# Kernel tuning notes

Hardware: AMD Instinct MI355X
Metric: run time of the kernel (lower is better)

Reference implementation:

```python
import jax, jax.numpy as jnp
import numpy as np


def setup_inputs() -> dict:
    key = jax.random.key(0)
    ks = jax.random.split(key, 7)
    n, L = 8, 1024
    s = 64            # input_size_1 = input_size_2 = 64
    d = s + 1         # 65, after bias-ones concat / h feature size
    inp = {
        "layer1": jax.random.normal(ks[0], (n, L, s), dtype=jnp.float32),
        "layer2": jax.random.normal(ks[1], (n, L, s), dtype=jnp.float32),
        "layer3": jax.random.normal(ks[2], (n, L, s), dtype=jnp.float32),
        "h1": jax.random.normal(ks[3], (n, L, d), dtype=jnp.float32),
        "h2": jax.random.normal(ks[4], (n, L, d), dtype=jnp.float32),
        "h3": jax.random.normal(ks[5], (n, L, d), dtype=jnp.float32),
        # quartic core W (xavier-normal-ish scale): shape (s1+1, s2+1, s2+1, s2+1)
        "W": jax.random.normal(ks[6], (d, d, d, d), dtype=jnp.float32) * 0.02,
    }
    return inp


def reference(layer1, layer2, layer3, h1, h2, h3, W):
    # Non-factorized, flag=True, 3D-input path of Qriaffine.forward:
    #   out = einsum('nia,abcd,njb,nic,njd->nij', [layer1;1], W, [layer2;1], h1, h2)
    # layer3 / h3 are unused in this branch (but layer3 is still concatenated
    # with ones in the original code, a no-op for the output).
    n, L, _ = layer1.shape
    ones = jnp.ones((n, L, 1), dtype=layer1.dtype)
    l1 = jnp.concatenate([layer1, ones], axis=-1)  # [n, L, d]
    l2 = jnp.concatenate([layer2, ones], axis=-1)  # [n, L, d]
    # efficient contraction order, avoiding the huge [n,L,d,d,d] intermediate:
    p = l1[..., :, None] * h1[..., None, :]          # niac: [n, L, d, d]
    q = jnp.einsum('niac,abcd->nibd', p, W)          # [n, L, d, d]
    r = l2[..., :, None] * h2[..., None, :]          # njbd: [n, L, d, d]
    out = jnp.einsum('nibd,njbd->nij', q, r)         # [n, L, L]
    return out
```

## Files before the change

kernel.cpp:

```cpp
#include <hip/hip_runtime.h>
#include <hip/hip_bf16.h>


typedef __attribute__((ext_vector_type(8))) short short8;
typedef __attribute__((ext_vector_type(16))) float floatx16;

#define KP 4288
#define DP 4352
#define NROW 8192

__device__ __forceinline__ void async_ld16(const void* g, void* l) {
  __builtin_amdgcn_global_load_lds(
      (const __attribute__((address_space(1))) unsigned int*)g,
      (__attribute__((address_space(3))) unsigned int*)l, 16, 0, 0);
}

__global__ void zero_kernel(float4* __restrict__ p, long n) {
  long i = (long)blockIdx.x * blockDim.x + threadIdx.x;
  long stride = (long)gridDim.x * blockDim.x;
  float4 z = make_float4(0.f, 0.f, 0.f, 0.f);
  for (; i < n; i += stride) p[i] = z;
}

__global__ void build_wt2(const float* __restrict__ W, __hip_bfloat16* __restrict__ Wt2) {
  __shared__ __hip_bfloat16 tile[65 * 66];
  const int a = blockIdx.x, b = blockIdx.y;
  const float* src = W + (size_t)(a * 65 + b) * 4225;
  for (int idx = threadIdx.x; idx < 4225; idx += 256) {
    int c = idx / 65, d = idx - c * 65;
    tile[d * 66 + c] = __float2bfloat16(src[idx]);
  }
  __syncthreads();
  for (int idx = threadIdx.x; idx < 4225; idx += 256) {
    int d = idx / 65, c = idx - d * 65;
    Wt2[(size_t)(b * 65 + d) * KP + a * 65 + c] = tile[d * 66 + c];
  }
}

__global__ void build_p(const float* __restrict__ layer, const float* __restrict__ h,
                        __hip_bfloat16* __restrict__ P, int width) {
  const int row = blockIdx.x;
  __shared__ float lv[65], hv[65];
  if (threadIdx.x < 64) lv[threadIdx.x] = layer[(size_t)row * 64 + threadIdx.x];
  if (threadIdx.x == 64) lv[64] = 1.0f;
  if (threadIdx.x < 65) hv[threadIdx.x] = h[(size_t)row * 65 + threadIdx.x];
  __syncthreads();
  for (int base = threadIdx.x * 8; base < width; base += 256 * 8) {
    alignas(16) __hip_bfloat16 tmp[8];
#pragma unroll
    for (int j = 0; j < 8; ++j) {
      int idx = base + j;
      float v = 0.f;
      if (idx < 4225) {
        int x = idx / 65, y = idx - x * 65;
        v = lv[x] * hv[y];
      }
      tmp[j] = __float2bfloat16(v);
    }
    *(float4*)(P + (size_t)row * width + base) = *(const float4*)tmp;
  }
}

template <int STORE_BF16>
__global__ __launch_bounds__(256) void gemm_nt(
    const __hip_bfloat16* __restrict__ A, const __hip_bfloat16* __restrict__ B,
    void* __restrict__ Cv, int K, int lda, int ldb, int ldc,
    long sA, long sB, long sC) {
  __shared__ alignas(16) __hip_bfloat16 As[128 * 64];
  __shared__ alignas(16) __hip_bfloat16 Bs[128 * 64];
  const int z = blockIdx.z;
  A += (long)z * sA;
  B += (long)z * sB;
  const int bm = blockIdx.y * 128;
  const int bn = blockIdx.x * 128;
  const int t = threadIdx.x;
  const int lane = t & 63;
  const int wave = t >> 6;
  const int l31 = lane & 31;
  const int lhi = lane >> 5;
  const int wm = (wave >> 1) * 64;
  const int wn = (wave & 1) * 64;

  const __hip_bfloat16* gA[4];
  const __hip_bfloat16* gB[4];
  __hip_bfloat16* lA[4];
  __hip_bfloat16* lB[4];
#pragma unroll
  for (int r = 0; r < 4; ++r) {
    int L = r * 256 + t;
    int row = L >> 3, sl = L & 7;
    int sg = sl ^ (row & 7);
    gA[r] = A + (size_t)(bm + row) * lda + sg * 8;
    gB[r] = B + (size_t)(bn + row) * ldb + sg * 8;
    lA[r] = As + (size_t)(r * 256 + wave * 64) * 8;
    lB[r] = Bs + (size_t)(r * 256 + wave * 64) * 8;
  }

  const int x7 = l31 & 7;
  const int rA0 = (wm + l31) * 64, rA1 = (wm + 32 + l31) * 64;
  const int rB0 = (wn + l31) * 64, rB1 = (wn + 32 + l31) * 64;

  floatx16 acc[2][2] = {};

  for (int k0 = 0; k0 < K; k0 += 64) {
    __syncthreads();
#pragma unroll
    for (int r = 0; r < 4; ++r) {
      async_ld16(gA[r] + k0, lA[r]);
      async_ld16(gB[r] + k0, lB[r]);
    }
    __syncthreads();

#pragma unroll
    for (int ks = 0; ks < 4; ++ks) {
      const int pc = ((ks * 2 + lhi) ^ x7) * 8;
      short8 a0 = *(const short8*)(&As[rA0 + pc]);
      short8 a1 = *(const short8*)(&As[rA1 + pc]);
      short8 b0 = *(const short8*)(&Bs[rB0 + pc]);
      short8 b1 = *(const short8*)(&Bs[rB1 + pc]);
      acc[0][0] = __builtin_amdgcn_mfma_f32_32x32x16_bf16(a0, b0, acc[0][0], 0, 0, 0);
      acc[0][1] = __builtin_amdgcn_mfma_f32_32x32x16_bf16(a0, b1, acc[0][1], 0, 0, 0);
      acc[1][0] = __builtin_amdgcn_mfma_f32_32x32x16_bf16(a1, b0, acc[1][0], 0, 0, 0);
      acc[1][1] = __builtin_amdgcn_mfma_f32_32x32x16_bf16(a1, b1, acc[1][1], 0, 0, 0);
    }
  }

  if (STORE_BF16) {
    __hip_bfloat16* C = (__hip_bfloat16*)Cv + (long)z * sC;
#pragma unroll
    for (int mt = 0; mt < 2; ++mt)
#pragma unroll
      for (int nt = 0; nt < 2; ++nt)
#pragma unroll
        for (int reg = 0; reg < 16; ++reg) {
          int row = bm + wm + mt * 32 + (reg & 3) + 8 * (reg >> 2) + 4 * lhi;
          int col = bn + wn + nt * 32 + l31;
          C[(size_t)row * ldc + col] = __float2bfloat16(acc[mt][nt][reg]);
        }
  } else {
    float* C = (float*)Cv + (long)z * sC;
#pragma unroll
    for (int mt = 0; mt < 2; ++mt)
#pragma unroll
      for (int nt = 0; nt < 2; ++nt)
#pragma unroll
        for (int reg = 0; reg < 16; ++reg) {
          int row = bm + wm + mt * 32 + (reg & 3) + 8 * (reg >> 2) + 4 * lhi;
          int col = bn + wn + nt * 32 + l31;
          C[(size_t)row * ldc + col] = acc[mt][nt][reg];
        }
  }
}

extern "C" void kernel_launch(void* const* d_in, const int* in_sizes, int n_in,
                              void* d_out, int out_size, void* d_ws, size_t ws_size,
                              hipStream_t stream) {
  const float* layer1 = (const float*)d_in[0];
  const float* layer2 = (const float*)d_in[1];
  const float* h1 = (const float*)d_in[3];
  const float* h2 = (const float*)d_in[4];
  const float* W = (const float*)d_in[6];
  float* out = (float*)d_out;

  char* ws = (char*)d_ws;
  __hip_bfloat16* P = (__hip_bfloat16*)(ws);
  __hip_bfloat16* Wt2 = (__hip_bfloat16*)(ws + 70254592ULL);
  __hip_bfloat16* Q = (__hip_bfloat16*)(ws + 107577344ULL);
  __hip_bfloat16* R = (__hip_bfloat16*)(ws);

  zero_kernel<<<2048, 256, 0, stream>>>((float4*)Wt2, (long)DP * KP * 2 / 16);
  build_wt2<<<dim3(65, 65), 256, 0, stream>>>(W, Wt2);
  build_p<<<NROW, 256, 0, stream>>>(layer1, h1, P, KP);
  gemm_nt<1><<<dim3(DP / 128, NROW / 128, 1), 256, 0, stream>>>(
      P, Wt2, Q, KP, KP, KP, DP, 0, 0, 0);
  build_p<<<NROW, 256, 0, stream>>>(layer2, h2, R, DP);
  gemm_nt<0><<<dim3(1024 / 128, 1024 / 128, 8), 256, 0, stream>>>(
      Q, R, out, DP, DP, DP, 1024, 1024L * DP, 1024L * DP, 1024L * 1024);
}
```

Measured before the change: 612.1 us.

## Pre-swizzle operands into MFMA fragment layout and load directly from global

```diff
diff --git a/kernel.cpp b/kernel.cpp
--- a/kernel.cpp
+++ b/kernel.cpp
@@ -8,12 +8,8 @@
 #define KP 4288
 #define DP 4352
 #define NROW 8192
-
-__device__ __forceinline__ void async_ld16(const void* g, void* l) {
-  __builtin_amdgcn_global_load_lds(
-      (const __attribute__((address_space(1))) unsigned int*)g,
-      (__attribute__((address_space(3))) unsigned int*)l, 16, 0, 0);
-}
+#define K16P 268
+#define K16D 272
 
 __global__ void zero_kernel(float4* __restrict__ p, long n) {
   long i = (long)blockIdx.x * blockDim.x + threadIdx.x;
@@ -22,123 +18,122 @@
   for (; i < n; i += stride) p[i] = z;
 }
 
-__global__ void build_wt2(const float* __restrict__ W, __hip_bfloat16* __restrict__ Wt2) {
-  __shared__ __hip_bfloat16 tile[65 * 66];
+__global__ void build_wt2f(const float* __restrict__ W, __hip_bfloat16* __restrict__ Bf) {
   const int a = blockIdx.x, b = blockIdx.y;
   const float* src = W + (size_t)(a * 65 + b) * 4225;
   for (int idx = threadIdx.x; idx < 4225; idx += 256) {
     int c = idx / 65, d = idx - c * 65;
-    tile[d * 66 + c] = __float2bfloat16(src[idx]);
-  }
-  __syncthreads();
-  for (int idx = threadIdx.x; idx < 4225; idx += 256) {
-    int d = idx / 65, c = idx - d * 65;
-    Wt2[(size_t)(b * 65 + d) * KP + a * 65 + c] = tile[d * 66 + c];
+    int bd = b * 65 + d;
+    int ac = a * 65 + c;
+    int lanef = (bd & 31) + ((ac >> 3) & 1) * 32;
+    size_t e = ((size_t)((bd >> 5) * K16P + (ac >> 4)) * 64 + lanef) * 8 + (ac & 7);
+    Bf[e] = __float2bfloat16(src[idx]);
   }
 }
 
-__global__ void build_p(const float* __restrict__ layer, const float* __restrict__ h,
-                        __hip_bfloat16* __restrict__ P, int width) {
-  const int row = blockIdx.x;
-  __shared__ float lv[65], hv[65];
-  if (threadIdx.x < 64) lv[threadIdx.x] = layer[(size_t)row * 64 + threadIdx.x];
-  if (threadIdx.x == 64) lv[64] = 1.0f;
-  if (threadIdx.x < 65) hv[threadIdx.x] = h[(size_t)row * 65 + threadIdx.x];
+__global__ void build_pf(const float* __restrict__ layer, const float* __restrict__ h,
+                         __hip_bfloat16* __restrict__ Pf, int K16) {
+  const int rb = blockIdx.x;
+  const int r0 = rb * 32;
+  __shared__ float lv[32][65];
+  __shared__ float hv[32][65];
+  const int t = threadIdx.x;
+  for (int i = t; i < 32 * 64; i += 256)
+    lv[i >> 6][i & 63] = layer[(size_t)(r0 + (i >> 6)) * 64 + (i & 63)];
+  if (t < 32) lv[t][64] = 1.0f;
+  for (int i = t; i < 32 * 65; i += 256) {
+    int rr = i / 65, y = i - rr * 65;
+    hv[rr][y] = h[(size_t)(r0 + rr) * 65 + y];
+  }
   __syncthreads();
-  for (int base = threadIdx.x * 8; base < width; base += 256 * 8) {
+  const int lane = t & 63;
+  const int rl = lane & 31;
+  const int kh = lane >> 5;
+  for (int kc = t >> 6; kc < K16; kc += 4) {
     alignas(16) __hip_bfloat16 tmp[8];
 #pragma unroll
-    for (int j = 0; j < 8; ++j) {
-      int idx = base + j;
+    for (int e = 0; e < 8; ++e) {
+      int k = kc * 16 + kh * 8 + e;
       float v = 0.f;
-      if (idx < 4225) {
-        int x = idx / 65, y = idx - x * 65;
-        v = lv[x] * hv[y];
+      if (k < 4225) {
+        int x = k / 65, y = k - x * 65;
+        v = lv[rl][x] * hv[rl][y];
       }
-      tmp[j] = __float2bfloat16(v);
+      tmp[e] = __float2bfloat16(v);
     }
-    *(float4*)(P + (size_t)row * width + base) = *(const float4*)tmp;
+    *(float4*)(Pf + ((size_t)(rb * K16 + kc) * 64 + lane) * 8) = *(const float4*)tmp;
   }
 }
 
-template <int STORE_BF16>
-__global__ __launch_bounds__(256) void gemm_nt(
+extern __shared__ char smem_[];
+template <int STORE_FRAG>
+__global__ __launch_bounds__(256, 2) void gemm_frag(
     const __hip_bfloat16* __restrict__ A, const __hip_bfloat16* __restrict__ B,
-    void* __restrict__ Cv, int K, int lda, int ldb, int ldc,
-    long sA, long sB, long sC) {
-  __shared__ alignas(16) __hip_bfloat16 As[128 * 64];
-  __shared__ alignas(16) __hip_bfloat16 Bs[128 * 64];
+    void* __restrict__ Cv, int K16, int cparam, long sA, long sB, long sC) {
   const int z = blockIdx.z;
-  A += (long)z * sA;
-  B += (long)z * sB;
-  const int bm = blockIdx.y * 128;
-  const int bn = blockIdx.x * 128;
+  const __hip_bfloat16* Ab = A + (size_t)z * sA;
+  const __hip_bfloat16* Bb = B + (size_t)z * sB;
   const int t = threadIdx.x;
   const int lane = t & 63;
   const int wave = t >> 6;
-  const int l31 = lane & 31;
-  const int lhi = lane >> 5;
-  const int wm = (wave >> 1) * 64;
-  const int wn = (wave & 1) * 64;
-
-  const __hip_bfloat16* gA[4];
-  const __hip_bfloat16* gB[4];
-  __hip_bfloat16* lA[4];
-  __hip_bfloat16* lB[4];
-#pragma unroll
-  for (int r = 0; r < 4; ++r) {
-    int L = r * 256 + t;
-    int row = L >> 3, sl = L & 7;
-    int sg = sl ^ (row & 7);
-    gA[r] = A + (size_t)(bm + row) * lda + sg * 8;
-    gB[r] = B + (size_t)(bn + row) * ldb + sg * 8;
-    lA[r] = As + (size_t)(r * 256 + wave * 64) * 8;
-    lB[r] = Bs + (size_t)(r * 256 + wave * 64) * 8;
-  }
-
-  const int x7 = l31 & 7;
-  const int rA0 = (wm + l31) * 64, rA1 = (wm + 32 + l31) * 64;
-  const int rB0 = (wn + l31) * 64, rB1 = (wn + 32 + l31) * 64;
+  const size_t rbA = (size_t)blockIdx.y * 4 + (wave >> 1) * 2;
+  const size_t rbB = (size_t)blockIdx.x * 4 + (wave & 1) * 2;
+  const __hip_bfloat16* pA0 = Ab + (rbA * K16 * 64 + lane) * 8;
+  const __hip_bfloat16* pA1 = pA0 + (size_t)K16 * 512;
+  const __hip_bfloat16* pB0 = Bb + (rbB * K16 * 64 + lane) * 8;
+  const __hip_bfloat16* pB1 = pB0 + (size_t)K16 * 512;
 
   floatx16 acc[2][2] = {};
 
-  for (int k0 = 0; k0 < K; k0 += 64) {
-    __syncthreads();
-#pragma unroll
-    for (int r = 0; r < 4; ++r) {
-      async_ld16(gA[r] + k0, lA[r]);
-      async_ld16(gB[r] + k0, lB[r]);
-    }
-    __syncthreads();
-
+  for (int kc = 0; kc < K16; kc += 4) {
+    const size_t off = (size_t)kc * 512;
+    short8 a0[4], a1[4], b0[4], b1[4];
 #pragma unroll
     for (int ks = 0; ks < 4; ++ks) {
-      const int pc = ((ks * 2 + lhi) ^ x7) * 8;
-      short8 a0 = *(const short8*)(&As[rA0 + pc]);
-      short8 a1 = *(const short8*)(&As[rA1 + pc]);
-      short8 b0 = *(const short8*)(&Bs[rB0 + pc]);
-      short8 b1 = *(const short8*)(&Bs[rB1 + pc]);
-      acc[0][0] = __builtin_amdgcn_mfma_f32_32x32x16_bf16(a0, b0, acc[0][0], 0, 0, 0);
-      acc[0][1] = __builtin_amdgcn_mfma_f32_32x32x16_bf16(a0, b1, acc[0][1], 0, 0, 0);
-      acc[1][0] = __builtin_amdgcn_mfma_f32_32x32x16_bf16(a1, b0, acc[1][0], 0, 0, 0);
-      acc[1][1] = __builtin_amdgcn_mfma_f32_32x32x16_bf16(a1, b1, acc[1][1], 0, 0, 0);
+      a0[ks] = *(const short8*)(pA0 + off + ks * 512);
+      a1[ks] = *(const short8*)(pA1 + off + ks * 512);
+      b0[ks] = *(const short8*)(pB0 + off + ks * 512);
+      b1[ks] = *(const short8*)(pB1 + off + ks * 512);
+    }
+#pragma unroll
+    for (int ks = 0; ks < 4; ++ks) {
+      acc[0][0] = __builtin_amdgcn_mfma_f32_32x32x16_bf16(a0[ks], b0[ks], acc[0][0], 0, 0, 0);
+      acc[0][1] = __builtin_amdgcn_mfma_f32_32x32x16_bf16(a0[ks], b1[ks], acc[0][1], 0, 0, 0);
+      acc[1][0] = __builtin_amdgcn_mfma_f32_32x32x16_bf16(a1[ks], b0[ks], acc[1][0], 0, 0, 0);
+      acc[1][1] = __builtin_amdgcn_mfma_f32_32x32x16_bf16(a1[ks], b1[ks], acc[1][1], 0, 0, 0);
     }
   }
 
-  if (STORE_BF16) {
-    __hip_bfloat16* C = (__hip_bfloat16*)Cv + (long)z * sC;
+  const int l31 = lane & 31, lhi = lane >> 5;
+  const int wm = (wave >> 1) * 64, wn = (wave & 1) * 64;
+  if (STORE_FRAG) {
+    __hip_bfloat16* lsq = (__hip_bfloat16*)smem_;
 #pragma unroll
     for (int mt = 0; mt < 2; ++mt)
 #pragma unroll
       for (int nt = 0; nt < 2; ++nt)
 #pragma unroll
         for (int reg = 0; reg < 16; ++reg) {
-          int row = bm + wm + mt * 32 + (reg & 3) + 8 * (reg >> 2) + 4 * lhi;
-          int col = bn + wn + nt * 32 + l31;
-          C[(size_t)row * ldc + col] = __float2bfloat16(acc[mt][nt][reg]);
+          int row = wm + mt * 32 + 4 * lhi + (reg & 3) + 8 * (reg >> 2);
+          int col = wn + nt * 32 + l31;
+          lsq[row * 136 + col] = __float2bfloat16(acc[mt][nt][reg]);
         }
+    __syncthreads();
+    __hip_bfloat16* Cq = (__hip_bfloat16*)Cv;
+    const int CK16 = cparam;
+#pragma unroll
+    for (int i = 0; i < 8; ++i) {
+      int f = wave * 8 + i;
+      int rbl = f >> 3, kcl = f & 7;
+      short8 v = *(const short8*)(&lsq[(rbl * 32 + l31) * 136 + kcl * 16 + lhi * 8]);
+      size_t rbQ = (size_t)blockIdx.y * 4 + rbl;
+      size_t kcQ = (size_t)blockIdx.x * 8 + kcl;
+      *(short8*)(Cq + (rbQ * CK16 + kcQ) * 512 + lane * 8) = v;
+    }
   } else {
-    float* C = (float*)Cv + (long)z * sC;
+    float* C = (float*)Cv + (size_t)z * sC;
+    const int ldc = cparam;
+    const int bm = blockIdx.y * 128, bn = blockIdx.x * 128;
 #pragma unroll
     for (int mt = 0; mt < 2; ++mt)
 #pragma unroll
@@ -163,17 +158,17 @@
   float* out = (float*)d_out;
 
   char* ws = (char*)d_ws;
-  __hip_bfloat16* P = (__hip_bfloat16*)(ws);
-  __hip_bfloat16* Wt2 = (__hip_bfloat16*)(ws + 70254592ULL);
-  __hip_bfloat16* Q = (__hip_bfloat16*)(ws + 107577344ULL);
-  __hip_bfloat16* R = (__hip_bfloat16*)(ws);
+  __hip_bfloat16* Pf = (__hip_bfloat16*)(ws);
+  __hip_bfloat16* Wt2f = (__hip_bfloat16*)(ws + 70254592ULL);
+  __hip_bfloat16* Qf = (__hip_bfloat16*)(ws + 107577344ULL);
+  __hip_bfloat16* Rf = (__hip_bfloat16*)(ws);
 
-  zero_kernel<<<2048, 256, 0, stream>>>((float4*)Wt2, (long)DP * KP * 2 / 16);
-  build_wt2<<<dim3(65, 65), 256, 0, stream>>>(W, Wt2);
-  build_p<<<NROW, 256, 0, stream>>>(layer1, h1, P, KP);
-  gemm_nt<1><<<dim3(DP / 128, NROW / 128, 1), 256, 0, stream>>>(
-      P, Wt2, Q, KP, KP, KP, DP, 0, 0, 0);
-  build_p<<<NROW, 256, 0, stream>>>(layer2, h2, R, DP);
-  gemm_nt<0><<<dim3(1024 / 128, 1024 / 128, 8), 256, 0, stream>>>(
-      Q, R, out, DP, DP, DP, 1024, 1024L * DP, 1024L * DP, 1024L * 1024);
+  zero_kernel<<<2048, 256, 0, stream>>>((float4*)Wt2f, 37044224LL / 16);
+  build_wt2f<<<dim3(65, 65), 256, 0, stream>>>(W, Wt2f);
+  build_pf<<<NROW / 32, 256, 0, stream>>>(layer1, h1, Pf, K16P);
+  gemm_frag<1><<<dim3(DP / 128, NROW / 128, 1), 256, 34816, stream>>>(
+      Pf, Wt2f, Qf, K16P, K16D, 0, 0, 0);
+  build_pf<<<NROW / 32, 256, 0, stream>>>(layer2, h2, Rf, K16D);
+  gemm_frag<0><<<dim3(1024 / 128, 1024 / 128, 8), 256, 0, stream>>>(
+      Qf, Rf, out, K16D, 1024, 1024L * DP, 1024L * DP, 1024L * 1024);
 }
```

Result: slower. 761.6 us (+24.4%).
